# Kernel tuning notes

Measured on AMD Instinct MI355X. Metric: run time of the kernel, lower is better.

Reference implementation:

```python
import jax, jax.numpy as jnp
import numpy as np

# ---- fixed analysis filters (pywt_coeffs) ----
GL = np.array([0.05441584224308161, 0.3128715909144659, 0.6756307362980128, 0.5853546836548691, -0.015829105256023893, -0.2840155429624281, 0.00047248457399797254, 0.128747426620186, -0.01736930100202211, -0.04408825393106472, 0.013981027917015516, 0.008746094047015655, -0.00487035299301066, -0.0003917403729959771, 0.0006754494059985568, -0.00011747678400228192])
GH = np.array([-0.00011747678400228192, -0.0006754494059985568, -0.0003917403729959771, 0.00487035299301066, 0.008746094047015655, -0.013981027917015516, -0.04408825393106472, 0.01736930100202211, 0.128747426620186, -0.00047248457399797254, -0.2840155429624281, 0.015829105256023893, 0.5853546836548691, -0.6756307362980128, 0.3128715909144659, -0.05441584224308161])

M2 = 8          # fix(16*0.5), half filter length
A_CUBIC = -0.75 # PyTorch bicubic coefficient


def _ihilbert(x):
    # scipy.fftpack.ihilbert: Fourier coeff y_j = -1j*sign(j)*x_j, y_0 = 0
    n = x.shape[0]
    signs = np.sign(np.fft.fftfreq(n))
    return np.real(np.fft.ifft(np.fft.fft(x) * (-1j) * signs))


def setup_inputs() -> dict:
    key = jax.random.key(0)
    k1, k2 = jax.random.split(key)
    LL = jax.random.normal(k1, (8, 32, 256, 256), dtype=jnp.float32)
    Yh0 = jax.random.normal(k2, (8, 32, 3, 256, 256), dtype=jnp.float32)
    gl = jnp.asarray(GL, dtype=jnp.float32)
    gh = jnp.asarray(GH, dtype=jnp.float32)
    fl = jnp.asarray(_ihilbert(GL), dtype=jnp.float32)
    fh = jnp.asarray(_ihilbert(GH), dtype=jnp.float32)
    return {"LL": LL, "Yh0": Yh0, "gl": gl, "gh": gh, "fl": fl, "fh": fh}


def _reflect_idx(n):
    # reflect(arange(-m2, n+m2), -0.5, n-0.5) -> half-sample reflected indices, length n+2*M2
    x = jnp.arange(-M2, n + M2, dtype=jnp.float32)
    rng = jnp.float32(n)  # (n-0.5) - (-0.5)
    mod = jnp.mod(x + 0.5, 2.0 * rng)
    out = jnp.where(mod >= rng, 2.0 * rng - mod, mod) - 0.5
    return out.astype(jnp.int32)


def colfilter(X, h):
    # Faithful to original: reflect-pad gather along rows, then the original
    # _column_convolve accumulates X*h[idx] WITHOUT shifting (source bug), which
    # equals X_ext * sum(h); the centered crop recovers the original rows.
    r = X.shape[2]
    xe = _reflect_idx(r)
    Y = X[:, :, xe, :] * jnp.sum(h)
    return Y[:, :, M2:M2 + r, :]


def rowfilter(X, h):
    c = X.shape[3]
    xe = _reflect_idx(c)
    Y = X[:, :, :, xe] * jnp.sum(h)
    return Y[:, :, :, M2:M2 + c]


def _cubic_kernel(d):
    d = jnp.abs(d)
    w1 = ((A_CUBIC + 2.0) * d - (A_CUBIC + 3.0)) * d * d + 1.0
    w2 = ((A_CUBIC * d - 5.0 * A_CUBIC) * d + 8.0 * A_CUBIC) * d - 4.0 * A_CUBIC
    return jnp.where(d <= 1.0, w1, jnp.where(d < 2.0, w2, 0.0))


def _up2_axis(X, axis):
    # PyTorch nn.Upsample(scale_factor=2, mode='bicubic', align_corners=False)
    n = X.shape[axis]
    i = jnp.arange(2 * n, dtype=jnp.float32)
    src = 0.5 * i - 0.25                      # (i+0.5)*in/out - 0.5
    f = jnp.floor(src)
    offs = jnp.arange(-1, 3, dtype=jnp.float32)
    pos = f[:, None] + offs[None, :]          # [2n, 4] tap positions
    idx = jnp.clip(pos, 0, n - 1).astype(jnp.int32)
    w = _cubic_kernel(src[:, None] - pos)     # [2n, 4]
    Xg = jnp.take(X, idx.reshape(-1), axis=axis)
    new_shape = X.shape[:axis] + (2 * n, 4) + X.shape[axis + 1:]
    Xg = Xg.reshape(new_shape)
    wb = w.reshape((1,) * axis + (2 * n, 4) + (1,) * (X.ndim - axis - 1))
    return jnp.sum(Xg * wb, axis=axis + 1)


def upsample2(X):
    return _up2_axis(_up2_axis(X, 2), 3)


def _iqwt(LL, Yh0, gl, gh, fl, fh):
    LH, HL, HH = Yh0[:, :, 0], Yh0[:, :, 1], Yh0[:, :, 2]
    s = LL.shape[1] // 4
    sp = lambda T: (T[:, 0:s], T[:, s:2 * s], T[:, 2 * s:3 * s], T[:, 3 * s:4 * s])
    lglg, lflg, lglf, lflf = sp(LL)
    lghg, lfhg, lghf, lfhf = sp(LH)
    hglg, hflg, hglf, hflf = sp(HL)
    hghg, hfhg, hghf, hfhf = sp(HH)

    # first component
    lghg_f = rowfilter(lghg, gh)  # reused below (original code bug)
    t = upsample2(rowfilter(lglg, gl)) + upsample2(lghg_f)
    t1 = colfilter(t, gl)
    t = upsample2(rowfilter(hglg, gl)) + upsample2(rowfilter(hghg, gh))
    first = t1 + colfilter(t, gh)

    # second component (note: original uses lghg_f, not rowfilter(lfhg, gh))
    t = upsample2(rowfilter(lflg, gl)) + upsample2(lghg_f)
    t1 = colfilter(t, fl)
    t = upsample2(rowfilter(hflg, gl)) + upsample2(rowfilter(hfhg, gh))
    second = t1 + colfilter(t, fh)

    # third component
    t = upsample2(rowfilter(lglf, fl)) + upsample2(rowfilter(lghf, fh))
    t1 = colfilter(t, gl)
    t = upsample2(rowfilter(hglf, fl)) + upsample2(rowfilter(hghf, fh))
    third = t1 + colfilter(t, gh)

    # fourth component
    t = upsample2(rowfilter(lflf, fl)) + upsample2(rowfilter(lfhf, fh))
    t1 = colfilter(t, fl)
    t = upsample2(rowfilter(hflf, fl)) + upsample2(rowfilter(hfhf, fh))
    fourth = t1 + colfilter(t, fh)

    y = first + second + third + fourth
    return (y - jnp.min(y)) / (jnp.max(y) - jnp.min(y))


def reference(LL, Yh0, gl, gh, fl, fh):
    return _iqwt(LL, Yh0, gl, gh, fl, fh)
```

## Files before the change

### kernel.cpp

```cpp
#include <hip/hip_runtime.h>

constexpr int IT  = 36;
constexpr int ITP = 37;
constexpr int STP = 68;

#define W0 (-0.03515625f)
#define W1 ( 0.26171875f)
#define W2 ( 0.87890625f)
#define W3 (-0.10546875f)

typedef float vfloat4 __attribute__((ext_vector_type(4)));

template <typename F>
__device__ __forceinline__ void tile_pipeline(
    const float* __restrict__ src, int tx, int ty, int t,
    float (&sIn)[IT][ITP], float (&sT)[IT][STP],
    float a0, float a1, float a2, float a3, int b0, int g, F&& consume)
{
    const int rin0 = ty * 32 - 2;
    const int cin0 = tx * 32 - 2;

    for (int idx = t; idx < IT * IT; idx += 256) {
        int r  = idx / IT;
        int cc = idx - r * IT;
        int gr = min(max(rin0 + r, 0), 255);
        int gc = min(max(cin0 + cc, 0), 255);
        sIn[r][cc] = src[gr * 256 + gc];
    }
    __syncthreads();

    for (int r = t >> 4; r < IT; r += 16) {
        float x0 = sIn[r][2 * g + 0];
        float x1 = sIn[r][2 * g + 1];
        float x2 = sIn[r][2 * g + 2];
        float x3 = sIn[r][2 * g + 3];
        float x4 = sIn[r][2 * g + 4];
        float x5 = sIn[r][2 * g + 5];
        vfloat4 v;
        v.x = W0 * x0 + W1 * x1 + W2 * x2 + W3 * x3;
        v.y = W3 * x1 + W2 * x2 + W1 * x3 + W0 * x4;
        v.z = W0 * x1 + W1 * x2 + W2 * x3 + W3 * x4;
        v.w = W3 * x2 + W2 * x3 + W1 * x4 + W0 * x5;
        *(vfloat4*)&sT[r][4 * g] = v;
    }
    __syncthreads();

#pragma unroll
    for (int it = 0; it < 4; ++it) {
        const int base = b0 + 8 * it;
        vfloat4 q0 = *(const vfloat4*)&sT[base + 0][4 * g];
        vfloat4 q1 = *(const vfloat4*)&sT[base + 1][4 * g];
        vfloat4 q2 = *(const vfloat4*)&sT[base + 2][4 * g];
        vfloat4 q3 = *(const vfloat4*)&sT[base + 3][4 * g];
        vfloat4 v = a0 * q0 + a1 * q1 + a2 * q2 + a3 * q3;
        consume(it, v);
    }
}

__device__ __forceinline__ void block_minmax(int t, float& mn, float& mx) {
    for (int off = 32; off > 0; off >>= 1) {
        mn = fminf(mn, __shfl_down(mn, off, 64));
        mx = fmaxf(mx, __shfl_down(mx, off, 64));
    }
    __shared__ float wmn[4], wmx[4];
    const int wv = t >> 6;
    if ((t & 63) == 0) { wmn[wv] = mn; wmx[wv] = mx; }
    __syncthreads();
    mn = fminf(fminf(wmn[0], wmn[1]), fminf(wmn[2], wmn[3]));
    mx = fmaxf(fmaxf(wmx[0], wmx[1]), fmaxf(wmx[2], wmx[3]));
}

__global__ __launch_bounds__(256)
void qwt_up(const float* __restrict__ LL, float* __restrict__ out,
            float* __restrict__ pmin, float* __restrict__ pmax)
{
    __shared__ float sIn[IT][ITP];
    __shared__ float sT[IT][STP];

    const int t  = threadIdx.x;
    const int tx = blockIdx.x;
    const int ty = blockIdx.y;
    const int pl = blockIdx.z;
    const float* src = LL + (size_t)((pl >> 3) * 32 + (pl & 7)) * (256 * 256);

    const int g  = t & 15;
    const int rs = t >> 4;
    const int od = rs & 1;
    const int b0 = (rs >> 1) + od;
    const float a0 = od ? W3 : W0;
    const float a1 = od ? W2 : W1;
    const float a2 = od ? W1 : W2;
    const float a3 = od ? W0 : W3;

    float* dst = out + (size_t)pl * (512 * 512)
               + (size_t)(ty * 64 + rs) * 512 + tx * 64 + 4 * g;

    float mn = 1e30f, mx = -1e30f;
    tile_pipeline(src, tx, ty, t, sIn, sT, a0, a1, a2, a3, b0, g,
        [&](int it, vfloat4 v) {
            mn = fminf(mn, fminf(fminf(v.x, v.y), fminf(v.z, v.w)));
            mx = fmaxf(mx, fmaxf(fmaxf(v.x, v.y), fmaxf(v.z, v.w)));
            *(vfloat4*)(dst + (size_t)(16 * it) * 512) = v;
        });

    block_minmax(t, mn, mx);
    if (t == 0) {
        const int p = (pl * 8 + ty) * 8 + tx;
        pmin[p] = mn;
        pmax[p] = mx;
    }
}

__global__ __launch_bounds__(256)
void qwt_reduce(const float* __restrict__ pmin,
                const float* __restrict__ pmax,
                float* __restrict__ res)
{
    const int t = threadIdx.x;
    float m = 1e30f, M = -1e30f;
#pragma unroll
    for (int k = 0; k < 16; ++k) {
        m = fminf(m, pmin[t + 256 * k]);
        M = fmaxf(M, pmax[t + 256 * k]);
    }
    block_minmax(t, m, M);
    if (t == 0) {
        res[0] = m;
        res[1] = 1.0f / (M - m);
    }
}

__global__ __launch_bounds__(256)
void qwt_norm(float* __restrict__ out, const float* __restrict__ res)
{
    const float sub = res[0];
    const float scl = res[1];

    constexpr size_t N4 = (size_t)64 * 512 * 512 / 4;
    vfloat4* p = (vfloat4*)out;

    size_t i = (size_t)blockIdx.x * 256 + threadIdx.x;
    const size_t stride = (size_t)gridDim.x * 256;
    for (size_t k = i; k < N4; k += stride) {
        vfloat4 v = p[k];
        __builtin_nontemporal_store((v - sub) * scl, &p[k]);
    }
}

extern "C" void kernel_launch(void* const* d_in, const int* in_sizes, int n_in,
                              void* d_out, int out_size, void* d_ws, size_t ws_size,
                              hipStream_t stream)
{
    (void)in_sizes; (void)n_in; (void)out_size; (void)ws_size;
    const float* LL = (const float*)d_in[0];
    float* out      = (float*)d_out;

    float* pmin = (float*)d_ws;
    float* pmax = pmin + 4096;
    float* res  = pmin + 8192;

    dim3 block(256);
    qwt_up<<<dim3(8, 8, 64), block, 0, stream>>>(LL, out, pmin, pmax);
    qwt_reduce<<<dim3(1), block, 0, stream>>>(pmin, pmax, res);
    qwt_norm<<<dim3(2048), block, 0, stream>>>(out, res);
}
```

Measured before the change: 304.2 us.

## Fuse upsample, min/max reduce and normalize into one cooperative persistent kernel

Replaces the three launches (upsample tile kernel, single-block reduce, normalize pass) with one cooperative kernel of 1024 persistent blocks. Each block processes four tiles, writes a per-block min/max, waits on a grid-wide sync, reduces all partials itself, then normalizes the tiles it wrote. This removes two launch gaps and the tiny serial reduce kernel, and the normalize pass rereads data the same block just wrote, which may still be in cache. The cost is a grid barrier that needs all blocks co-resident, less parallelism per tile phase, and a redundant 1024-entry reduction done by every block.

```diff
diff --git a/kernel.cpp b/kernel.cpp
--- a/kernel.cpp
+++ b/kernel.cpp
@@ -1,4 +1,7 @@
 #include <hip/hip_runtime.h>
+#include <hip/hip_cooperative_groups.h>
+
+namespace cg = cooperative_groups;
 
 constexpr int IT  = 36;
 constexpr int ITP = 37;
@@ -10,6 +13,9 @@
 #define W3 (-0.10546875f)
 
 typedef float vfloat4 __attribute__((ext_vector_type(4)));
+
+constexpr int NBLK  = 1024;
+constexpr int TILES = 4096;
 
 template <typename F>
 __device__ __forceinline__ void tile_pipeline(
@@ -71,17 +77,14 @@
 }
 
 __global__ __launch_bounds__(256)
-void qwt_up(const float* __restrict__ LL, float* __restrict__ out,
-            float* __restrict__ pmin, float* __restrict__ pmax)
+void qwt_fused(const float* __restrict__ LL, float* __restrict__ out,
+               float* __restrict__ pmin, float* __restrict__ pmax)
 {
     __shared__ float sIn[IT][ITP];
     __shared__ float sT[IT][STP];
 
-    const int t  = threadIdx.x;
-    const int tx = blockIdx.x;
-    const int ty = blockIdx.y;
-    const int pl = blockIdx.z;
-    const float* src = LL + (size_t)((pl >> 3) * 32 + (pl & 7)) * (256 * 256);
+    const int t = threadIdx.x;
+    const int b = blockIdx.x;
 
     const int g  = t & 15;
     const int rs = t >> 4;
@@ -92,58 +95,55 @@
     const float a2 = od ? W1 : W2;
     const float a3 = od ? W0 : W3;
 
-    float* dst = out + (size_t)pl * (512 * 512)
-               + (size_t)(ty * 64 + rs) * 512 + tx * 64 + 4 * g;
+    float mn = 1e30f, mx = -1e30f;
 
-    float mn = 1e30f, mx = -1e30f;
-    tile_pipeline(src, tx, ty, t, sIn, sT, a0, a1, a2, a3, b0, g,
-        [&](int it, vfloat4 v) {
-            mn = fminf(mn, fminf(fminf(v.x, v.y), fminf(v.z, v.w)));
-            mx = fmaxf(mx, fmaxf(fmaxf(v.x, v.y), fmaxf(v.z, v.w)));
-            *(vfloat4*)(dst + (size_t)(16 * it) * 512) = v;
-        });
+#pragma unroll
+    for (int i = 0; i < TILES / NBLK; ++i) {
+        const int tau = b + NBLK * i;
+        const int tx = tau & 7;
+        const int ty = (tau >> 3) & 7;
+        const int pl = tau >> 6;
+        const float* src = LL + (size_t)((pl >> 3) * 32 + (pl & 7)) * (256 * 256);
+        float* dst = out + (size_t)pl * (512 * 512)
+                   + (size_t)(ty * 64 + rs) * 512 + tx * 64 + 4 * g;
+
+        tile_pipeline(src, tx, ty, t, sIn, sT, a0, a1, a2, a3, b0, g,
+            [&](int it, vfloat4 v) {
+                mn = fminf(mn, fminf(fminf(v.x, v.y), fminf(v.z, v.w)));
+                mx = fmaxf(mx, fmaxf(fmaxf(v.x, v.y), fmaxf(v.z, v.w)));
+                *(vfloat4*)(dst + (size_t)(16 * it) * 512) = v;
+            });
+    }
 
     block_minmax(t, mn, mx);
-    if (t == 0) {
-        const int p = (pl * 8 + ty) * 8 + tx;
-        pmin[p] = mn;
-        pmax[p] = mx;
-    }
-}
+    if (t == 0) { pmin[b] = mn; pmax[b] = mx; }
 
-__global__ __launch_bounds__(256)
-void qwt_reduce(const float* __restrict__ pmin,
-                const float* __restrict__ pmax,
-                float* __restrict__ res)
-{
-    const int t = threadIdx.x;
+    cg::this_grid().sync();
+
     float m = 1e30f, M = -1e30f;
 #pragma unroll
-    for (int k = 0; k < 16; ++k) {
+    for (int k = 0; k < NBLK / 256; ++k) {
         m = fminf(m, pmin[t + 256 * k]);
         M = fmaxf(M, pmax[t + 256 * k]);
     }
     block_minmax(t, m, M);
-    if (t == 0) {
-        res[0] = m;
-        res[1] = 1.0f / (M - m);
-    }
-}
+    const float sub = m;
+    const float scl = 1.0f / (M - m);
 
-__global__ __launch_bounds__(256)
-void qwt_norm(float* __restrict__ out, const float* __restrict__ res)
-{
-    const float sub = res[0];
-    const float scl = res[1];
-
-    constexpr size_t N4 = (size_t)64 * 512 * 512 / 4;
-    vfloat4* p = (vfloat4*)out;
-
-    size_t i = (size_t)blockIdx.x * 256 + threadIdx.x;
-    const size_t stride = (size_t)gridDim.x * 256;
-    for (size_t k = i; k < N4; k += stride) {
-        vfloat4 v = p[k];
-        __builtin_nontemporal_store((v - sub) * scl, &p[k]);
+#pragma unroll
+    for (int i = 0; i < TILES / NBLK; ++i) {
+        const int tau = b + NBLK * i;
+        const int tx = tau & 7;
+        const int ty = (tau >> 3) & 7;
+        const int pl = tau >> 6;
+        float* dst = out + (size_t)pl * (512 * 512)
+                   + (size_t)(ty * 64 + rs) * 512 + tx * 64 + 4 * g;
+#pragma unroll
+        for (int it = 0; it < 4; ++it) {
+            vfloat4 v = *(vfloat4*)(dst + (size_t)(16 * it) * 512);
+            __builtin_nontemporal_store((v - sub) * scl,
+                                        (vfloat4*)(dst + (size_t)(16 * it) * 512));
+        }
     }
 }
 
@@ -156,11 +156,9 @@
     float* out      = (float*)d_out;
 
     float* pmin = (float*)d_ws;
-    float* pmax = pmin + 4096;
-    float* res  = pmin + 8192;
+    float* pmax = pmin + NBLK;
 
-    dim3 block(256);
-    qwt_up<<<dim3(8, 8, 64), block, 0, stream>>>(LL, out, pmin, pmax);
-    qwt_reduce<<<dim3(1), block, 0, stream>>>(pmin, pmax, res);
-    qwt_norm<<<dim3(2048), block, 0, stream>>>(out, res);
+    void* args[] = { (void*)&LL, (void*)&out, (void*)&pmin, (void*)&pmax };
+    hipLaunchCooperativeKernel((void*)qwt_fused, dim3(NBLK), dim3(256),
+                               args, 0, stream);
 }
```

Result: slower. 426.5 us (+40.2%).
